# Kernel tuning notes

Measured on AMD Instinct MI355X. Metric: run time of the kernel, lower is better.

Reference implementation:

```python
import jax, jax.numpy as jnp
import numpy as np

N_NODES = 50000
N_EDGES = 800000
D_FEAT = 64
N_CLASS = 2


def spmm(edge_src, edge_dst, edge_val, x, num_nodes):
    # out[d] = sum_{e: dst[e]=d} val[e] * x[src[e]]  == sparse adj @ x (COO)
    msgs = x[edge_src] * edge_val[:, None]  # [E, F]
    return jax.ops.segment_sum(msgs, edge_dst, num_segments=num_nodes)


def setup_inputs() -> dict:
    key = jax.random.key(0)
    ks = jax.random.split(key, 6)
    x = jax.random.normal(ks[0], (N_NODES, D_FEAT), dtype=jnp.float32)
    edge_src = jax.random.randint(ks[1], (N_EDGES,), 0, N_NODES, dtype=jnp.int32)
    edge_dst = jax.random.randint(ks[2], (N_EDGES,), 0, N_NODES, dtype=jnp.int32)
    edge_val = jax.random.uniform(ks[3], (N_EDGES,), dtype=jnp.float32)
    fc_w = jax.random.normal(ks[4], (N_CLASS, D_FEAT), dtype=jnp.float32) / np.sqrt(D_FEAT)
    fc_b = jax.random.normal(ks[5], (N_CLASS,), dtype=jnp.float32) * 0.01
    return {"x": x, "edge_src": edge_src, "edge_dst": edge_dst,
            "edge_val": edge_val, "fc_w": fc_w, "fc_b": fc_b}


def reference(x, edge_src, edge_dst, edge_val, fc_w, fc_b):
    # gc1: x = adj @ x  (no weights in lightGCN conv layer)
    h = spmm(edge_src, edge_dst, edge_val, x, N_NODES)
    # gc2: second propagation hop
    h = spmm(edge_src, edge_dst, edge_val, h, N_NODES)
    # fc: nn.Linear(nfeat, nclass)
    logits = h @ fc_w.T + fc_b  # [N, nclass]
    return jax.nn.log_softmax(logits, axis=1)
```

## Files before the change

### kernel.cpp

```cpp
#include <hip/hip_runtime.h>
#include <hip/hip_bf16.h>

#define N_NODES 50000
#define N_EDGES 800000
#define D_FEAT 64

#define NBUCK 196
#define CHUNK 8192
#define NB ((N_EDGES + CHUNK - 1) / CHUNK)
#define NT (NBUCK * NB)
#define NPB ((NT + 255) / 256)
#define BSTAG 6144
#define CVTB ((N_NODES * D_FEAT / 4 + 1023) / 1024)

#define VAL_DEQ (1.0f / 65535.0f)

__device__ __forceinline__ unsigned short f2b(float f) {
    unsigned int u = __float_as_uint(f);
    unsigned int lsb = (u >> 16) & 1u;
    u += 0x7fffu + lsb;
    return (unsigned short)(u >> 16);
}
__device__ __forceinline__ float blo(unsigned int u) { return __uint_as_float(u << 16); }
__device__ __forceinline__ float bhi(unsigned int u) { return __uint_as_float(u & 0xffff0000u); }

__global__ __launch_bounds__(1024) void cvt_hist_kernel(const float* __restrict__ x,
                                                        unsigned short* __restrict__ xb,
                                                        const int* __restrict__ dst,
                                                        int* __restrict__ counts) {
    __shared__ int h[NBUCK];
    int t = threadIdx.x;
    if (blockIdx.x < NB) {
        int blk = blockIdx.x;
        for (int i = t; i < NBUCK; i += 1024) h[i] = 0;
        __syncthreads();
        int e0 = blk * CHUNK;
        int ce = min(CHUNK, N_EDGES - e0);
        for (int k = 0; k < CHUNK / 1024; ++k) {
            int i = t + k * 1024;
            if (i < ce) atomicAdd(&h[dst[e0 + i] >> 8], 1);
        }
        __syncthreads();
        for (int i = t; i < NBUCK; i += 1024) counts[i * NB + blk] = h[i];
    } else {
        int i = (blockIdx.x - NB) * 1024 + t;
        if (i < (N_NODES * D_FEAT) / 4) {
            float4 v = reinterpret_cast<const float4*>(x)[i];
            ushort4 o;
            o.x = f2b(v.x); o.y = f2b(v.y); o.z = f2b(v.z); o.w = f2b(v.w);
            reinterpret_cast<ushort4*>(xb)[i] = o;
        }
    }
}

__global__ void scanA_block_kernel(const int* __restrict__ counts,
                                   int* __restrict__ pre,
                                   int* __restrict__ partials) {
    __shared__ int sm[256];
    int i = blockIdx.x * 256 + threadIdx.x;
    int v = (i < NT) ? counts[i] : 0;
    sm[threadIdx.x] = v;
    __syncthreads();
    for (int off = 1; off < 256; off <<= 1) {
        int t2 = (threadIdx.x >= (unsigned)off) ? sm[threadIdx.x - off] : 0;
        __syncthreads();
        sm[threadIdx.x] += t2;
        __syncthreads();
    }
    if (i < NT) pre[i] = sm[threadIdx.x] - v;
    if (threadIdx.x == 255) partials[blockIdx.x] = sm[threadIdx.x];
}

__global__ __launch_bounds__(1024) void partition_kernel(const int* __restrict__ src,
                                                         const int* __restrict__ dst,
                                                         const float* __restrict__ val,
                                                         const int* __restrict__ counts,
                                                         const int* __restrict__ pre,
                                                         const int* __restrict__ partials,
                                                         int2* __restrict__ pack) {
    __shared__ int2 stag[CHUNK];
    __shared__ int  hist[NBUCK];
    __shared__ int  basearr[NBUCK];
    __shared__ int  cur[NBUCK];
    __shared__ int  sboff[NBUCK];
    __shared__ int  sc[256];
    __shared__ int  psc[256];
    __shared__ int  exc[256];
    int t = threadIdx.x, blk = blockIdx.x;
    int e0 = blk * CHUNK;
    int ce = min(CHUNK, N_EDGES - e0);

    for (int i = t; i < NBUCK; i += 1024) hist[i] = counts[i * NB + blk];
    int myp = 0;
    if (t < 256) {
        myp = (t < NPB) ? partials[t] : 0;
        psc[t] = myp;
    }
    __syncthreads();
    for (int off = 1; off < 256; off <<= 1) {
        int v = 0;
        if (t < 256 && t >= off) v = psc[t - off];
        __syncthreads();
        if (t < 256) psc[t] += v;
        __syncthreads();
    }
    if (t < 256) exc[t] = psc[t] - myp;
    if (t < 256) sc[t] = (t < NBUCK) ? hist[t] : 0;
    __syncthreads();
    for (int off = 1; off < 256; off <<= 1) {
        int v = 0;
        if (t < 256 && t >= off) v = sc[t - off];
        __syncthreads();
        if (t < 256) sc[t] += v;
        __syncthreads();
    }
    if (t < NBUCK) {
        int excl = sc[t] - hist[t];
        basearr[t] = excl;
        cur[t] = excl;
        int idx = t * NB + blk;
        sboff[t] = pre[idx] + exc[idx >> 8];
    }
    __syncthreads();
    for (int k = 0; k < CHUNK / 1024; ++k) {
        int i = t + k * 1024;
        if (i < ce) {
            int e = e0 + i;
            int d = dst[e];
            int b = d >> 8;
            int slot = atomicAdd(&cur[b], 1);
            stag[slot] = make_int2((src[e] & 0xffff) | ((d & 255) << 16) | (b << 24),
                                   __float_as_int(val[e]));
        }
    }
    __syncthreads();
    for (int k = 0; k < CHUNK / 1024; ++k) {
        int i = t + k * 1024;
        if (i < ce) {
            int2 p = stag[i];
            int b = ((unsigned)p.x) >> 24;
            pack[sboff[b] + (i - basearr[b])] = p;
        }
    }
}

__global__ __launch_bounds__(1024) void bucket_sort_kernel(const int2* __restrict__ pack,
                                                           const int* __restrict__ pre,
                                                           const int* __restrict__ partials,
                                                           unsigned int* __restrict__ packc,
                                                           int* __restrict__ row_ptr) {
    __shared__ int2     stag[BSTAG];
    __shared__ unsigned sorted[BSTAG];
    __shared__ int cnt[256];
    __shared__ int sc[256];
    __shared__ int cur[256];
    __shared__ int psc[256];
    __shared__ int esee[2];
    int t = threadIdx.x, b = blockIdx.x;

    int myp = 0;
    if (t < 256) {
        myp = (t < NPB) ? partials[t] : 0;
        psc[t] = myp;
        cnt[t] = 0;
    }
    __syncthreads();
    for (int off = 1; off < 256; off <<= 1) {
        int v = 0;
        if (t < 256 && t >= off) v = psc[t - off];
        __syncthreads();
        if (t < 256) psc[t] += v;
        __syncthreads();
    }
    if (t < 256) psc[t] -= myp;
    __syncthreads();
    if (t == 0) {
        int i0 = b * NB;
        esee[0] = pre[i0] + psc[i0 >> 8];
        if (b == NBUCK - 1) esee[1] = N_EDGES;
        else {
            int i1 = (b + 1) * NB;
            esee[1] = pre[i1] + psc[i1 >> 8];
        }
    }
    __syncthreads();
    int es = esee[0];
    int ce = min(esee[1] - es, BSTAG);

    for (int k = 0; k < BSTAG / 1024; ++k) {
        int i = t + k * 1024;
        if (i < ce) {
            int2 p = pack[es + i];
            stag[i] = p;
            atomicAdd(&cnt[(p.x >> 16) & 255], 1);
        }
    }
    __syncthreads();
    if (t < 256) sc[t] = cnt[t];
    __syncthreads();
    for (int off = 1; off < 256; off <<= 1) {
        int v = 0;
        if (t < 256 && t >= off) v = sc[t - off];
        __syncthreads();
        if (t < 256) sc[t] += v;
        __syncthreads();
    }
    if (t < 256) {
        int excl = sc[t] - cnt[t];
        cur[t] = excl;
        int node = (b << 8) + t;
        if (node < N_NODES) row_ptr[node] = es + excl;
        if (b == NBUCK - 1 && t == 0) row_ptr[N_NODES] = N_EDGES;
    }
    __syncthreads();
    for (int k = 0; k < BSTAG / 1024; ++k) {
        int i = t + k * 1024;
        if (i < ce) {
            int2 p = stag[i];
            int d = (p.x >> 16) & 255;
            int slot = atomicAdd(&cur[d], 1);
            float v = __int_as_float(p.y);
            unsigned q = (unsigned)(v * 65535.0f + 0.5f);
            sorted[slot] = (unsigned)(p.x & 0xffff) | (q << 16);
        }
    }
    __syncthreads();
    for (int k = 0; k < BSTAG / 1024; ++k) {
        int i = t + k * 1024;
        if (i < ce) packc[es + i] = sorted[i];
    }
}

__global__ void spmm_gather_kernel(const int* __restrict__ row_ptr,
                                   const unsigned int* __restrict__ packc,
                                   const unsigned short* __restrict__ xb,
                                   unsigned short* __restrict__ hb) {
    int t = blockIdx.x * blockDim.x + threadIdx.x;
    int node = t >> 3;
    if (node >= N_NODES) return;
    int c = (t & 7) << 3;
    int beg = row_ptr[node];
    int end = row_ptr[node + 1];
    float a0 = 0.f, a1 = 0.f, a2 = 0.f, a3 = 0.f, a4 = 0.f, a5 = 0.f, a6 = 0.f, a7 = 0.f;
    int j = beg;
    for (; j + 3 < end; j += 4) {
        unsigned p0 = packc[j], p1 = packc[j + 1], p2 = packc[j + 2], p3 = packc[j + 3];
        uint4 q0 = *reinterpret_cast<const uint4*>(xb + (long)(p0 & 0xffffu) * D_FEAT + c);
        uint4 q1 = *reinterpret_cast<const uint4*>(xb + (long)(p1 & 0xffffu) * D_FEAT + c);
        uint4 q2 = *reinterpret_cast<const uint4*>(xb + (long)(p2 & 0xffffu) * D_FEAT + c);
        uint4 q3 = *reinterpret_cast<const uint4*>(xb + (long)(p3 & 0xffffu) * D_FEAT + c);
        float v0 = (float)(p0 >> 16) * VAL_DEQ;
        float v1 = (float)(p1 >> 16) * VAL_DEQ;
        float v2 = (float)(p2 >> 16) * VAL_DEQ;
        float v3 = (float)(p3 >> 16) * VAL_DEQ;
        a0 += v0 * blo(q0.x) + v1 * blo(q1.x) + v2 * blo(q2.x) + v3 * blo(q3.x);
        a1 += v0 * bhi(q0.x) + v1 * bhi(q1.x) + v2 * bhi(q2.x) + v3 * bhi(q3.x);
        a2 += v0 * blo(q0.y) + v1 * blo(q1.y) + v2 * blo(q2.y) + v3 * blo(q3.y);
        a3 += v0 * bhi(q0.y) + v1 * bhi(q1.y) + v2 * bhi(q2.y) + v3 * bhi(q3.y);
        a4 += v0 * blo(q0.z) + v1 * blo(q1.z) + v2 * blo(q2.z) + v3 * blo(q3.z);
        a5 += v0 * bhi(q0.z) + v1 * bhi(q1.z) + v2 * bhi(q2.z) + v3 * bhi(q3.z);
        a6 += v0 * blo(q0.w) + v1 * blo(q1.w) + v2 * blo(q2.w) + v3 * blo(q3.w);
        a7 += v0 * bhi(q0.w) + v1 * bhi(q1.w) + v2 * bhi(q2.w) + v3 * bhi(q3.w);
    }
    for (; j < end; ++j) {
        unsigned p0 = packc[j];
        uint4 q0 = *reinterpret_cast<const uint4*>(xb + (long)(p0 & 0xffffu) * D_FEAT + c);
        float v0 = (float)(p0 >> 16) * VAL_DEQ;
        a0 += v0 * blo(q0.x); a1 += v0 * bhi(q0.x);
        a2 += v0 * blo(q0.y); a3 += v0 * bhi(q0.y);
        a4 += v0 * blo(q0.z); a5 += v0 * bhi(q0.z);
        a6 += v0 * blo(q0.w); a7 += v0 * bhi(q0.w);
    }
    uint4 o;
    o.x = (unsigned)f2b(a0) | ((unsigned)f2b(a1) << 16);
    o.y = (unsigned)f2b(a2) | ((unsigned)f2b(a3) << 16);
    o.z = (unsigned)f2b(a4) | ((unsigned)f2b(a5) << 16);
    o.w = (unsigned)f2b(a6) | ((unsigned)f2b(a7) << 16);
    *reinterpret_cast<uint4*>(hb + (long)node * D_FEAT + c) = o;
}

__global__ void spmm_fc_fused_kernel(const int* __restrict__ row_ptr,
                                     const unsigned int* __restrict__ packc,
                                     const unsigned short* __restrict__ hb,
                                     const float* __restrict__ w,
                                     const float* __restrict__ b,
                                     float* __restrict__ out) {
    int t = blockIdx.x * blockDim.x + threadIdx.x;
    int node = t >> 3;
    if (node >= N_NODES) return;
    int lane = t & 7;
    int c = lane << 3;
    int beg = row_ptr[node];
    int end = row_ptr[node + 1];
    float a0 = 0.f, a1 = 0.f, a2 = 0.f, a3 = 0.f, a4 = 0.f, a5 = 0.f, a6 = 0.f, a7 = 0.f;
    int j = beg;
    for (; j + 3 < end; j += 4) {
        unsigned p0 = packc[j], p1 = packc[j + 1], p2 = packc[j + 2], p3 = packc[j + 3];
        uint4 q0 = *reinterpret_cast<const uint4*>(hb + (long)(p0 & 0xffffu) * D_FEAT + c);
        uint4 q1 = *reinterpret_cast<const uint4*>(hb + (long)(p1 & 0xffffu) * D_FEAT + c);
        uint4 q2 = *reinterpret_cast<const uint4*>(hb + (long)(p2 & 0xffffu) * D_FEAT + c);
        uint4 q3 = *reinterpret_cast<const uint4*>(hb + (long)(p3 & 0xffffu) * D_FEAT + c);
        float v0 = (float)(p0 >> 16) * VAL_DEQ;
        float v1 = (float)(p1 >> 16) * VAL_DEQ;
        float v2 = (float)(p2 >> 16) * VAL_DEQ;
        float v3 = (float)(p3 >> 16) * VAL_DEQ;
        a0 += v0 * blo(q0.x) + v1 * blo(q1.x) + v2 * blo(q2.x) + v3 * blo(q3.x);
        a1 += v0 * bhi(q0.x) + v1 * bhi(q1.x) + v2 * bhi(q2.x) + v3 * bhi(q3.x);
        a2 += v0 * blo(q0.y) + v1 * blo(q1.y) + v2 * blo(q2.y) + v3 * blo(q3.y);
        a3 += v0 * bhi(q0.y) + v1 * bhi(q1.y) + v2 * bhi(q2.y) + v3 * bhi(q3.y);
        a4 += v0 * blo(q0.z) + v1 * blo(q1.z) + v2 * blo(q2.z) + v3 * blo(q3.z);
        a5 += v0 * bhi(q0.z) + v1 * bhi(q1.z) + v2 * bhi(q2.z) + v3 * bhi(q3.z);
        a6 += v0 * blo(q0.w) + v1 * blo(q1.w) + v2 * blo(q2.w) + v3 * blo(q3.w);
        a7 += v0 * bhi(q0.w) + v1 * bhi(q1.w) + v2 * bhi(q2.w) + v3 * bhi(q3.w);
    }
    for (; j < end; ++j) {
        unsigned p0 = packc[j];
        uint4 q0 = *reinterpret_cast<const uint4*>(hb + (long)(p0 & 0xffffu) * D_FEAT + c);
        float v0 = (float)(p0 >> 16) * VAL_DEQ;
        a0 += v0 * blo(q0.x); a1 += v0 * bhi(q0.x);
        a2 += v0 * blo(q0.y); a3 += v0 * bhi(q0.y);
        a4 += v0 * blo(q0.z); a5 += v0 * bhi(q0.z);
        a6 += v0 * blo(q0.w); a7 += v0 * bhi(q0.w);
    }
    const float4 wa0 = *reinterpret_cast<const float4*>(w + c);
    const float4 wa1 = *reinterpret_cast<const float4*>(w + c + 4);
    const float4 wb0 = *reinterpret_cast<const float4*>(w + D_FEAT + c);
    const float4 wb1 = *reinterpret_cast<const float4*>(w + D_FEAT + c + 4);
    float p0 = a0 * wa0.x + a1 * wa0.y + a2 * wa0.z + a3 * wa0.w
             + a4 * wa1.x + a5 * wa1.y + a6 * wa1.z + a7 * wa1.w;
    float p1 = a0 * wb0.x + a1 * wb0.y + a2 * wb0.z + a3 * wb0.w
             + a4 * wb1.x + a5 * wb1.y + a6 * wb1.z + a7 * wb1.w;
#pragma unroll
    for (int off = 4; off >= 1; off >>= 1) {
        p0 += __shfl_down(p0, off, 8);
        p1 += __shfl_down(p1, off, 8);
    }
    if (lane == 0) {
        float acc0 = p0 + b[0];
        float acc1 = p1 + b[1];
        float m = fmaxf(acc0, acc1);
        float lse = m + logf(expf(acc0 - m) + expf(acc1 - m));
        out[(long)node * 2 + 0] = acc0 - lse;
        out[(long)node * 2 + 1] = acc1 - lse;
    }
}

extern "C" void kernel_launch(void* const* d_in, const int* in_sizes, int n_in,
                              void* d_out, int out_size, void* d_ws, size_t ws_size,
                              hipStream_t stream) {
    const float* x        = (const float*)d_in[0];
    const int*   edge_src = (const int*)d_in[1];
    const int*   edge_dst = (const int*)d_in[2];
    const float* edge_val = (const float*)d_in[3];
    const float* fc_w     = (const float*)d_in[4];
    const float* fc_b     = (const float*)d_in[5];
    float* out = (float*)d_out;

    const size_t tab_elems = (size_t)N_NODES * D_FEAT;
    unsigned short* xb      = (unsigned short*)d_ws;
    unsigned short* hb      = xb + tab_elems;
    int2*           pack    = (int2*)(hb + tab_elems);
    unsigned int*   packc   = (unsigned int*)(pack + N_EDGES);
    int*            counts  = (int*)(packc + N_EDGES);
    int*            pre     = counts + NT;
    int*            partials= pre + NT;
    int*            row_ptr = partials + NPB;

    cvt_hist_kernel<<<NB + CVTB, 1024, 0, stream>>>(x, xb, edge_dst, counts);
    scanA_block_kernel<<<NPB, 256, 0, stream>>>(counts, pre, partials);
    partition_kernel<<<NB, 1024, 0, stream>>>(edge_src, edge_dst, edge_val,
                                              counts, pre, partials, pack);
    bucket_sort_kernel<<<NBUCK, 1024, 0, stream>>>(pack, pre, partials, packc, row_ptr);

    const int threads_spmm = N_NODES * 8;
    dim3 grid_spmm((threads_spmm + 255) / 256);
    spmm_gather_kernel<<<grid_spmm, 256, 0, stream>>>(row_ptr, packc, xb, hb);

    spmm_fc_fused_kernel<<<grid_spmm, 256, 0, stream>>>(
        row_ptr, packc, hb, fc_w, fc_b, out);
}
```

Baseline: 61.17 us.

## Split bf16 feature tables into two 32-column planes for cache-resident gathers

The bf16 feature table is stored as two separate planes of 32 features each, and each SpMM hop runs as two passes, one per plane. Each plane is 3.2MB instead of 6.4MB, so the random row gathers are more likely to hit in L2. The cost is reading the CSR index array twice per hop, two extra kernel launches, and a float2 scratch buffer that holds the partial FC result between the two final passes.

```diff
diff --git a/kernel.cpp b/kernel.cpp
--- a/kernel.cpp
+++ b/kernel.cpp
@@ -4,6 +4,7 @@
 #define N_NODES 50000
 #define N_EDGES 800000
 #define D_FEAT 64
+#define PLANE 32
 
 #define NBUCK 196
 #define CHUNK 8192
@@ -25,7 +26,8 @@
 __device__ __forceinline__ float bhi(unsigned int u) { return __uint_as_float(u & 0xffff0000u); }
 
 __global__ __launch_bounds__(1024) void cvt_hist_kernel(const float* __restrict__ x,
-                                                        unsigned short* __restrict__ xb,
+                                                        unsigned short* __restrict__ xb0,
+                                                        unsigned short* __restrict__ xb1,
                                                         const int* __restrict__ dst,
                                                         int* __restrict__ counts) {
     __shared__ int h[NBUCK];
@@ -48,7 +50,11 @@
             float4 v = reinterpret_cast<const float4*>(x)[i];
             ushort4 o;
             o.x = f2b(v.x); o.y = f2b(v.y); o.z = f2b(v.z); o.w = f2b(v.w);
-            reinterpret_cast<ushort4*>(xb)[i] = o;
+            int flat = i << 2;
+            int node = flat >> 6;
+            int f = flat & 63;
+            unsigned short* p = (f < PLANE) ? xb0 : xb1;
+            *reinterpret_cast<ushort4*>(p + node * PLANE + (f & 31)) = o;
         }
     }
 }
@@ -231,24 +237,24 @@
     }
 }
 
-__global__ void spmm_gather_kernel(const int* __restrict__ row_ptr,
-                                   const unsigned int* __restrict__ packc,
-                                   const unsigned short* __restrict__ xb,
-                                   unsigned short* __restrict__ hb) {
+__global__ void spmm_gather_plane_kernel(const int* __restrict__ row_ptr,
+                                         const unsigned int* __restrict__ packc,
+                                         const unsigned short* __restrict__ xp,
+                                         unsigned short* __restrict__ hp) {
     int t = blockIdx.x * blockDim.x + threadIdx.x;
     int node = t >> 3;
     if (node >= N_NODES) return;
-    int c = (t & 7) << 3;
+    int c = (t & 7) << 2;
     int beg = row_ptr[node];
     int end = row_ptr[node + 1];
-    float a0 = 0.f, a1 = 0.f, a2 = 0.f, a3 = 0.f, a4 = 0.f, a5 = 0.f, a6 = 0.f, a7 = 0.f;
+    float a0 = 0.f, a1 = 0.f, a2 = 0.f, a3 = 0.f;
     int j = beg;
     for (; j + 3 < end; j += 4) {
         unsigned p0 = packc[j], p1 = packc[j + 1], p2 = packc[j + 2], p3 = packc[j + 3];
-        uint4 q0 = *reinterpret_cast<const uint4*>(xb + (long)(p0 & 0xffffu) * D_FEAT + c);
-        uint4 q1 = *reinterpret_cast<const uint4*>(xb + (long)(p1 & 0xffffu) * D_FEAT + c);
-        uint4 q2 = *reinterpret_cast<const uint4*>(xb + (long)(p2 & 0xffffu) * D_FEAT + c);
-        uint4 q3 = *reinterpret_cast<const uint4*>(xb + (long)(p3 & 0xffffu) * D_FEAT + c);
+        uint2 q0 = *reinterpret_cast<const uint2*>(xp + (p0 & 0xffffu) * PLANE + c);
+        uint2 q1 = *reinterpret_cast<const uint2*>(xp + (p1 & 0xffffu) * PLANE + c);
+        uint2 q2 = *reinterpret_cast<const uint2*>(xp + (p2 & 0xffffu) * PLANE + c);
+        uint2 q3 = *reinterpret_cast<const uint2*>(xp + (p3 & 0xffffu) * PLANE + c);
         float v0 = (float)(p0 >> 16) * VAL_DEQ;
         float v1 = (float)(p1 >> 16) * VAL_DEQ;
         float v2 = (float)(p2 >> 16) * VAL_DEQ;
@@ -257,49 +263,44 @@
         a1 += v0 * bhi(q0.x) + v1 * bhi(q1.x) + v2 * bhi(q2.x) + v3 * bhi(q3.x);
         a2 += v0 * blo(q0.y) + v1 * blo(q1.y) + v2 * blo(q2.y) + v3 * blo(q3.y);
         a3 += v0 * bhi(q0.y) + v1 * bhi(q1.y) + v2 * bhi(q2.y) + v3 * bhi(q3.y);
-        a4 += v0 * blo(q0.z) + v1 * blo(q1.z) + v2 * blo(q2.z) + v3 * blo(q3.z);
-        a5 += v0 * bhi(q0.z) + v1 * bhi(q1.z) + v2 * bhi(q2.z) + v3 * bhi(q3.z);
-        a6 += v0 * blo(q0.w) + v1 * blo(q1.w) + v2 * blo(q2.w) + v3 * blo(q3.w);
-        a7 += v0 * bhi(q0.w) + v1 * bhi(q1.w) + v2 * bhi(q2.w) + v3 * bhi(q3.w);
     }
     for (; j < end; ++j) {
         unsigned p0 = packc[j];
-        uint4 q0 = *reinterpret_cast<const uint4*>(xb + (long)(p0 & 0xffffu) * D_FEAT + c);
+        uint2 q0 = *reinterpret_cast<const uint2*>(xp + (p0 & 0xffffu) * PLANE + c);
         float v0 = (float)(p0 >> 16) * VAL_DEQ;
         a0 += v0 * blo(q0.x); a1 += v0 * bhi(q0.x);
         a2 += v0 * blo(q0.y); a3 += v0 * bhi(q0.y);
-        a4 += v0 * blo(q0.z); a5 += v0 * bhi(q0.z);
-        a6 += v0 * blo(q0.w); a7 += v0 * bhi(q0.w);
-    }
-    uint4 o;
+    }
+    uint2 o;
     o.x = (unsigned)f2b(a0) | ((unsigned)f2b(a1) << 16);
     o.y = (unsigned)f2b(a2) | ((unsigned)f2b(a3) << 16);
-    o.z = (unsigned)f2b(a4) | ((unsigned)f2b(a5) << 16);
-    o.w = (unsigned)f2b(a6) | ((unsigned)f2b(a7) << 16);
-    *reinterpret_cast<uint4*>(hb + (long)node * D_FEAT + c) = o;
-}
-
-__global__ void spmm_fc_fused_kernel(const int* __restrict__ row_ptr,
+    *reinterpret_cast<uint2*>(hp + node * PLANE + c) = o;
+}
+
+__global__ void spmm_fc_plane_kernel(const int* __restrict__ row_ptr,
                                      const unsigned int* __restrict__ packc,
-                                     const unsigned short* __restrict__ hb,
+                                     const unsigned short* __restrict__ hp,
                                      const float* __restrict__ w,
                                      const float* __restrict__ b,
-                                     float* __restrict__ out) {
+                                     float2* __restrict__ pp,
+                                     float* __restrict__ out,
+                                     int phase) {
     int t = blockIdx.x * blockDim.x + threadIdx.x;
     int node = t >> 3;
     if (node >= N_NODES) return;
     int lane = t & 7;
-    int c = lane << 3;
+    int c = lane << 2;
+    int po = phase * PLANE;
     int beg = row_ptr[node];
     int end = row_ptr[node + 1];
-    float a0 = 0.f, a1 = 0.f, a2 = 0.f, a3 = 0.f, a4 = 0.f, a5 = 0.f, a6 = 0.f, a7 = 0.f;
+    float a0 = 0.f, a1 = 0.f, a2 = 0.f, a3 = 0.f;
     int j = beg;
     for (; j + 3 < end; j += 4) {
         unsigned p0 = packc[j], p1 = packc[j + 1], p2 = packc[j + 2], p3 = packc[j + 3];
-        uint4 q0 = *reinterpret_cast<const uint4*>(hb + (long)(p0 & 0xffffu) * D_FEAT + c);
-        uint4 q1 = *reinterpret_cast<const uint4*>(hb + (long)(p1 & 0xffffu) * D_FEAT + c);
-        uint4 q2 = *reinterpret_cast<const uint4*>(hb + (long)(p2 & 0xffffu) * D_FEAT + c);
-        uint4 q3 = *reinterpret_cast<const uint4*>(hb + (long)(p3 & 0xffffu) * D_FEAT + c);
+        uint2 q0 = *reinterpret_cast<const uint2*>(hp + (p0 & 0xffffu) * PLANE + c);
+        uint2 q1 = *reinterpret_cast<const uint2*>(hp + (p1 & 0xffffu) * PLANE + c);
+        uint2 q2 = *reinterpret_cast<const uint2*>(hp + (p2 & 0xffffu) * PLANE + c);
+        uint2 q3 = *reinterpret_cast<const uint2*>(hp + (p3 & 0xffffu) * PLANE + c);
         float v0 = (float)(p0 >> 16) * VAL_DEQ;
         float v1 = (float)(p1 >> 16) * VAL_DEQ;
         float v2 = (float)(p2 >> 16) * VAL_DEQ;
@@ -308,40 +309,35 @@
         a1 += v0 * bhi(q0.x) + v1 * bhi(q1.x) + v2 * bhi(q2.x) + v3 * bhi(q3.x);
         a2 += v0 * blo(q0.y) + v1 * blo(q1.y) + v2 * blo(q2.y) + v3 * blo(q3.y);
         a3 += v0 * bhi(q0.y) + v1 * bhi(q1.y) + v2 * bhi(q2.y) + v3 * bhi(q3.y);
-        a4 += v0 * blo(q0.z) + v1 * blo(q1.z) + v2 * blo(q2.z) + v3 * blo(q3.z);
-        a5 += v0 * bhi(q0.z) + v1 * bhi(q1.z) + v2 * bhi(q2.z) + v3 * bhi(q3.z);
-        a6 += v0 * blo(q0.w) + v1 * blo(q1.w) + v2 * blo(q2.w) + v3 * blo(q3.w);
-        a7 += v0 * bhi(q0.w) + v1 * bhi(q1.w) + v2 * bhi(q2.w) + v3 * bhi(q3.w);
     }
     for (; j < end; ++j) {
         unsigned p0 = packc[j];
-        uint4 q0 = *reinterpret_cast<const uint4*>(hb + (long)(p0 & 0xffffu) * D_FEAT + c);
+        uint2 q0 = *reinterpret_cast<const uint2*>(hp + (p0 & 0xffffu) * PLANE + c);
         float v0 = (float)(p0 >> 16) * VAL_DEQ;
         a0 += v0 * blo(q0.x); a1 += v0 * bhi(q0.x);
         a2 += v0 * blo(q0.y); a3 += v0 * bhi(q0.y);
-        a4 += v0 * blo(q0.z); a5 += v0 * bhi(q0.z);
-        a6 += v0 * blo(q0.w); a7 += v0 * bhi(q0.w);
-    }
-    const float4 wa0 = *reinterpret_cast<const float4*>(w + c);
-    const float4 wa1 = *reinterpret_cast<const float4*>(w + c + 4);
-    const float4 wb0 = *reinterpret_cast<const float4*>(w + D_FEAT + c);
-    const float4 wb1 = *reinterpret_cast<const float4*>(w + D_FEAT + c + 4);
-    float p0 = a0 * wa0.x + a1 * wa0.y + a2 * wa0.z + a3 * wa0.w
-             + a4 * wa1.x + a5 * wa1.y + a6 * wa1.z + a7 * wa1.w;
-    float p1 = a0 * wb0.x + a1 * wb0.y + a2 * wb0.z + a3 * wb0.w
-             + a4 * wb1.x + a5 * wb1.y + a6 * wb1.z + a7 * wb1.w;
+    }
+    const float4 w0v = *reinterpret_cast<const float4*>(w + po + c);
+    const float4 w1v = *reinterpret_cast<const float4*>(w + D_FEAT + po + c);
+    float p0 = a0 * w0v.x + a1 * w0v.y + a2 * w0v.z + a3 * w0v.w;
+    float p1 = a0 * w1v.x + a1 * w1v.y + a2 * w1v.z + a3 * w1v.w;
 #pragma unroll
     for (int off = 4; off >= 1; off >>= 1) {
         p0 += __shfl_down(p0, off, 8);
         p1 += __shfl_down(p1, off, 8);
     }
     if (lane == 0) {
-        float acc0 = p0 + b[0];
-        float acc1 = p1 + b[1];
-        float m = fmaxf(acc0, acc1);
-        float lse = m + logf(expf(acc0 - m) + expf(acc1 - m));
-        out[(long)node * 2 + 0] = acc0 - lse;
-        out[(long)node * 2 + 1] = acc1 - lse;
+        if (phase == 0) {
+            pp[node] = make_float2(p0, p1);
+        } else {
+            float2 prev = pp[node];
+            float acc0 = prev.x + p0 + b[0];
+            float acc1 = prev.y + p1 + b[1];
+            float m = fmaxf(acc0, acc1);
+            float lse = m + logf(expf(acc0 - m) + expf(acc1 - m));
+            out[(long)node * 2 + 0] = acc0 - lse;
+            out[(long)node * 2 + 1] = acc1 - lse;
+        }
     }
 }
 
@@ -356,17 +352,20 @@
     const float* fc_b     = (const float*)d_in[5];
     float* out = (float*)d_out;
 
-    const size_t tab_elems = (size_t)N_NODES * D_FEAT;
-    unsigned short* xb      = (unsigned short*)d_ws;
-    unsigned short* hb      = xb + tab_elems;
-    int2*           pack    = (int2*)(hb + tab_elems);
+    const size_t plane_elems = (size_t)N_NODES * PLANE;
+    unsigned short* xb0     = (unsigned short*)d_ws;
+    unsigned short* xb1     = xb0 + plane_elems;
+    unsigned short* hb0     = xb1 + plane_elems;
+    unsigned short* hb1     = hb0 + plane_elems;
+    int2*           pack    = (int2*)(hb1 + plane_elems);
     unsigned int*   packc   = (unsigned int*)(pack + N_EDGES);
     int*            counts  = (int*)(packc + N_EDGES);
     int*            pre     = counts + NT;
     int*            partials= pre + NT;
     int*            row_ptr = partials + NPB;
-
-    cvt_hist_kernel<<<NB + CVTB, 1024, 0, stream>>>(x, xb, edge_dst, counts);
+    float2*         pp      = (float2*)(row_ptr + N_NODES + 1);
+
+    cvt_hist_kernel<<<NB + CVTB, 1024, 0, stream>>>(x, xb0, xb1, edge_dst, counts);
     scanA_block_kernel<<<NPB, 256, 0, stream>>>(counts, pre, partials);
     partition_kernel<<<NB, 1024, 0, stream>>>(edge_src, edge_dst, edge_val,
                                               counts, pre, partials, pack);
@@ -374,8 +373,10 @@
 
     const int threads_spmm = N_NODES * 8;
     dim3 grid_spmm((threads_spmm + 255) / 256);
-    spmm_gather_kernel<<<grid_spmm, 256, 0, stream>>>(row_ptr, packc, xb, hb);
-
-    spmm_fc_fused_kernel<<<grid_spmm, 256, 0, stream>>>(
-        row_ptr, packc, hb, fc_w, fc_b, out);
-}
+    spmm_gather_plane_kernel<<<grid_spmm, 256, 0, stream>>>(row_ptr, packc, xb0, hb0);
+    spmm_gather_plane_kernel<<<grid_spmm, 256, 0, stream>>>(row_ptr, packc, xb1, hb1);
+    spmm_fc_plane_kernel<<<grid_spmm, 256, 0, stream>>>(row_ptr, packc, hb0,
+                                                        fc_w, fc_b, pp, out, 0);
+    spmm_fc_plane_kernel<<<grid_spmm, 256, 0, stream>>>(row_ptr, packc, hb1,
+                                                        fc_w, fc_b, pp, out, 1);
+}
```

Measured after the change: 79.09 us. 29.3% more time.
